# Optimization experiments

Hardware: AMD Instinct MI355X
Metric: run time of the kernel (lower is better)

## Reference

```python
import jax, jax.numpy as jnp
import numpy as np

D_MODEL = 2048
D_STATE = 64
D_HEAD = 64
EXPAND = 2
CHUNK = 256
D_INNER = EXPAND * D_MODEL          # 4096
N_HEADS = D_INNER // D_HEAD          # 64
PARAM_DIM = 1 + 2 * D_STATE          # 129


def setup_inputs() -> dict:
    key = jax.random.key(0)
    k0, k1, k2, k3 = jax.random.split(key, 4)
    x = jax.random.normal(k0, (1, 4096, D_MODEL), jnp.float32)
    w_in = jax.random.normal(k1, (2 * D_INNER, D_MODEL), jnp.float32) * 0.02
    w_param = jax.random.normal(k2, (N_HEADS * PARAM_DIM, D_MODEL), jnp.float32) * 0.02
    w_out = jax.random.normal(k3, (D_MODEL, D_INNER), jnp.float32) * 0.02
    return {"x": x, "w_in": w_in, "w_param": w_param, "w_out": w_out}


def _ssd(a, Bm, Cm, X, Q):
    # a: (nb, l), Bm/Cm: (nb, l, ds), X: (nb, l, dh). Mamba-2 SSD chunked scan.
    nb, l = a.shape
    ds = Bm.shape[-1]
    dh = X.shape[-1]
    nc = l // Q
    la = jnp.log(a).reshape(nb, nc, Q)
    cs = jnp.cumsum(la, axis=-1)                      # cumulative log-decay within chunk
    Bc = Bm.reshape(nb, nc, Q, ds)
    Cc = Cm.reshape(nb, nc, Q, ds)
    Xc = X.reshape(nb, nc, Q, dh)
    # intra-chunk (attention-like dual): L[i,j] = prod_{r=j+1..i} a_r, j<=i
    tri = jnp.tril(jnp.ones((Q, Q), bool))
    L = jnp.where(tri, jnp.exp(cs[..., :, None] - cs[..., None, :]), 0.0)
    scores = jnp.einsum('znid,znjd->znij', Cc, Bc) * L
    y_diag = jnp.einsum('znij,znjh->znih', scores, Xc)
    # per-chunk state contribution: sum_j decay_to_end[j] * B_j^T x_j -> (nb,nc,ds,dh)
    decay_states = jnp.exp(cs[..., -1:] - cs)
    states = jnp.einsum('znj,znjd,znjh->zndh', decay_states, Bc, Xc)
    A_chunk = jnp.exp(cs[..., -1])                    # total decay per chunk (nb, nc)
    def step(S, inp):
        Ac, st = inp
        S_prev = S
        return Ac[:, None, None] * S + st, S_prev
    S0 = jnp.zeros((nb, ds, dh), a.dtype)
    _, S_prev = jax.lax.scan(step, S0, (A_chunk.T, jnp.moveaxis(states, 1, 0)))
    S_prev = jnp.moveaxis(S_prev, 0, 1)               # state entering each chunk (nb,nc,ds,dh)
    y_inter = jnp.einsum('znid,zndh,zni->znih', Cc, S_prev, jnp.exp(cs))
    return (y_diag + y_inter).reshape(nb, l, dh)


def reference(x, w_in, w_param, w_out):
    b, l, _ = x.shape
    xr = x @ w_in.T                                   # (b, l, 2*d_inner)
    inp, res = xr[..., :D_INNER], xr[..., D_INNER:]
    params = (x @ w_param.T).reshape(b, l, N_HEADS, PARAM_DIM)
    dt = jax.nn.softplus(params[..., 0])
    a = jnp.exp(-dt)                                  # (b, l, n_heads)
    Bp = params[..., 1:1 + D_STATE]
    Cp = params[..., 1 + D_STATE:]
    nb = b * N_HEADS
    # NOTE: raw row-major reshapes, mirroring the torch source exactly
    y = _ssd(a.reshape(nb, l),
             Bp.reshape(nb, l, D_STATE),
             Cp.reshape(nb, l, D_STATE),
             inp.reshape(nb, l, D_HEAD),
             CHUNK)
    y = y.reshape(b, l, D_INNER)
    out = y * jax.nn.silu(res)
    return out @ w_out.T
```

## Files before the change

### kernel.cpp

```cpp
#include <hip/hip_runtime.h>
#include <math.h>

#define Q 256

typedef unsigned short u16;
typedef unsigned int u32;
typedef __attribute__((ext_vector_type(8))) short short8;
typedef __attribute__((ext_vector_type(4))) float f32x4;

__device__ __forceinline__ float bf2f(u32 u){
  union { float f; u32 i; } v; v.i = u << 16; return v.f;
}
__device__ __forceinline__ u16 f2bf(float f){
  union { float f; u32 i; } v; v.f = f;
  u32 r = (v.i + 0x7FFFu + ((v.i >> 16) & 1u)) >> 16;
  return (u16)r;
}
__device__ __forceinline__ float softplusf(float x){
  return x > 20.f ? x : log1pf(expf(x));
}
__device__ __forceinline__ float siluf(float x){
  return x / (1.f + expf(-x));
}

__device__ __forceinline__ void gload_lds16(const void* g, const void* l){
  __builtin_amdgcn_global_load_lds(
    (const __attribute__((address_space(1))) void*)(uintptr_t)g,
    (__attribute__((address_space(3))) void*)(u32)(uintptr_t)l,
    16, 0, 0);
}

__device__ __forceinline__ u32 swz_off(int row, int col2){
  return (u32)(row*128 + (col2 ^ ((row & 7) << 4)));
}
__device__ __forceinline__ short8 frag_ld(const u16* buf, int row, int kk, int lk){
  return *(const short8*)((const char*)buf + row*128 + (((kk*4 + lk) ^ (row & 7)) << 4));
}

__global__ __launch_bounds__(256) void cast_bf16(const float* __restrict__ in,
    u16* __restrict__ out)
{
  const size_t i = ((size_t)blockIdx.x * 256 + threadIdx.x) * 4;
  const float4 v = *(const float4*)(in + i);
  ushort4 o;
  o.x = f2bf(v.x); o.y = f2bf(v.y); o.z = f2bf(v.z); o.w = f2bf(v.w);
  *(ushort4*)(out + i) = o;
}

#define MFMA_GEMM_CORE(Abf_, Bbf_, K_) \
  __shared__ short As[128*64]; \
  __shared__ short Bs[128*64]; \
  const int tid = threadIdx.x; \
  const int w = tid >> 6, l = tid & 63; \
  const int m0 = blockIdx.y * 128, n0 = blockIdx.x * 128; \
  const int wr = (w >> 1) * 64, wc = (w & 1) * 64; \
  const int sub = l >> 3; \
  const int scol = ((l & 7) ^ sub) * 8; \
  const int lr16 = l & 15; \
  const int koff = (l >> 4) << 4; \
  const int swz = (l & 7) << 4; \
  f32x4 acc[4][4]; \
  { f32x4 z = {0.f, 0.f, 0.f, 0.f}; \
    _Pragma("unroll") for (int m_ = 0; m_ < 4; m_++) \
    _Pragma("unroll") for (int n_ = 0; n_ < 4; n_++) acc[m_][n_] = z; } \
  const u16* Agp = (Abf_) + (size_t)m0 * (K_); \
  const u16* Bgp = (Bbf_) + (size_t)n0 * (K_); \
  for (int kt = 0; kt < (K_); kt += 64) { \
    __syncthreads(); \
    _Pragma("unroll") for (int i_ = 0; i_ < 4; i_++) { \
      const int rbase = i_*32 + w*8; \
      gload_lds16(Agp + (size_t)(rbase + sub)*(K_) + kt + scol, As + rbase*64); \
      gload_lds16(Bgp + (size_t)(rbase + sub)*(K_) + kt + scol, Bs + rbase*64); \
    } \
    __syncthreads(); \
    short8 af[2][4], bf[2][4]; \
    _Pragma("unroll") for (int kk = 0; kk < 2; kk++) { \
      _Pragma("unroll") for (int m_ = 0; m_ < 4; m_++) \
        af[kk][m_] = *(const short8*)((const char*)As + (wr + m_*16 + lr16)*128 + ((kk*64 + koff) ^ swz)); \
      _Pragma("unroll") for (int n_ = 0; n_ < 4; n_++) \
        bf[kk][n_] = *(const short8*)((const char*)Bs + (wc + n_*16 + lr16)*128 + ((kk*64 + koff) ^ swz)); \
    } \
    _Pragma("unroll") for (int m_ = 0; m_ < 4; m_++) \
    _Pragma("unroll") for (int n_ = 0; n_ < 4; n_++) \
    _Pragma("unroll") for (int kk = 0; kk < 2; kk++) \
      acc[m_][n_] = __builtin_amdgcn_mfma_f32_16x16x32_bf16(af[kk][m_], bf[kk][n_], acc[m_][n_], 0, 0, 0); \
  } \
  const int orow0 = m0 + wr + ((l >> 4) << 2); \
  const int ocol0 = n0 + wc + (l & 15);

__global__ __launch_bounds__(256) void gemm_in(const u16* __restrict__ A,
    const u16* __restrict__ B, u16* __restrict__ inp, u16* __restrict__ resb)
{
  MFMA_GEMM_CORE(A, B, 2048)
  #pragma unroll
  for (int m_ = 0; m_ < 4; m_++)
    #pragma unroll
    for (int n_ = 0; n_ < 4; n_++) {
      const int col = ocol0 + n_*16;
      #pragma unroll
      for (int j = 0; j < 4; j++) {
        const int row = orow0 + m_*16 + j;
        const u16 v = f2bf(acc[m_][n_][j]);
        if (col < 4096) inp[(size_t)row*4096 + col] = v;
        else            resb[(size_t)row*4096 + (col - 4096)] = v;
      }
    }
}

__global__ __launch_bounds__(256) void gemm_par(const u16* __restrict__ A,
    const u16* __restrict__ B, float* __restrict__ dtb,
    u16* __restrict__ Bb, u16* __restrict__ Cb)
{
  MFMA_GEMM_CORE(A, B, 2048)
  #pragma unroll
  for (int m_ = 0; m_ < 4; m_++)
    #pragma unroll
    for (int n_ = 0; n_ < 4; n_++) {
      const int col = ocol0 + n_*16;
      if (col < 8256) {
        const int h = col / 129, rr = col - h*129;
        #pragma unroll
        for (int j = 0; j < 4; j++) {
          const int row = orow0 + m_*16 + j;
          const float v = acc[m_][n_][j];
          if (rr == 0)      dtb[(size_t)row*64 + h] = v;
          else if (rr < 65) Bb[((size_t)row*64 + h)*64 + (rr-1)]  = f2bf(v);
          else              Cb[((size_t)row*64 + h)*64 + (rr-65)] = f2bf(v);
        }
      }
    }
}

__global__ __launch_bounds__(256) void gemm_out(const u16* __restrict__ A,
    const u16* __restrict__ B, float* __restrict__ C)
{
  MFMA_GEMM_CORE(A, B, 4096)
  #pragma unroll
  for (int m_ = 0; m_ < 4; m_++)
    #pragma unroll
    for (int n_ = 0; n_ < 4; n_++) {
      const int col = ocol0 + n_*16;
      #pragma unroll
      for (int j = 0; j < 4; j++)
        C[(size_t)(orow0 + m_*16 + j)*2048 + col] = acc[m_][n_][j];
    }
}

__global__ __launch_bounds__(256) void ssd_phaseA(const float* __restrict__ dtb,
    const u16* __restrict__ Bb, const u16* __restrict__ inp,
    float* __restrict__ cs_g, float* __restrict__ achunk, float* __restrict__ states_t)
{
  const int g = blockIdx.x, tid = threadIdx.x;
  const int p = g * Q + tid;
  __shared__ float sc[Q];
  __shared__ u16 sBt[64*64];
  __shared__ u16 sXt[64*64];
  sc[tid] = -softplusf(dtb[p]);
  __syncthreads();
  for (int off = 1; off < Q; off <<= 1) {
    float v = (tid >= off) ? sc[tid - off] : 0.f;
    __syncthreads();
    if (tid >= off) sc[tid] += v;
    __syncthreads();
  }
  cs_g[p] = sc[tid];
  const float cl = sc[Q-1];
  if (tid == 0) achunk[g] = expf(cl);

  const int w = tid >> 6, l = tid & 63;
  const int lrow = l & 15, lk = l >> 4;
  const int tj = tid & 63, tcb = (tid >> 6) * 16;
  f32x4 acc[4];
  { f32x4 z = {0,0,0,0}; acc[0]=z; acc[1]=z; acc[2]=z; acc[3]=z; }

  for (int js = 0; js < 4; js++) {
    __syncthreads();
    {
      const int jc = js*64 + tj;
      const float wj = expf(cl - sc[jc]);
      const size_t prow = ((size_t)g*Q + jc) * 64;
      union { uint4 v; u16 s[8]; } b0, b1, x0, x1;
      b0.v = *(const uint4*)&Bb[prow + tcb];
      b1.v = *(const uint4*)&Bb[prow + tcb + 8];
      x0.v = *(const uint4*)&inp[prow + tcb];
      x1.v = *(const uint4*)&inp[prow + tcb + 8];
      #pragma unroll
      for (int q = 0; q < 8; q++) {
        const int r0 = tcb + q, r1 = tcb + 8 + q;
        *(u16*)((char*)sBt + swz_off(r0, 2*tj)) = f2bf(wj * bf2f((u32)b0.s[q]));
        *(u16*)((char*)sBt + swz_off(r1, 2*tj)) = f2bf(wj * bf2f((u32)b1.s[q]));
        *(u16*)((char*)sXt + swz_off(r0, 2*tj)) = x0.s[q];
        *(u16*)((char*)sXt + swz_off(r1, 2*tj)) = x1.s[q];
      }
    }
    __syncthreads();
    short8 aX0 = frag_ld(sXt, w*16 + lrow, 0, lk);
    short8 aX1 = frag_ld(sXt, w*16 + lrow, 1, lk);
    #pragma unroll
    for (int n = 0; n < 4; n++) {
      short8 b0 = frag_ld(sBt, n*16 + lrow, 0, lk);
      short8 b1 = frag_ld(sBt, n*16 + lrow, 1, lk);
      acc[n] = __builtin_amdgcn_mfma_f32_16x16x32_bf16(aX0, b0, acc[n], 0, 0, 0);
      acc[n] = __builtin_amdgcn_mfma_f32_16x16x32_bf16(aX1, b1, acc[n], 0, 0, 0);
    }
  }
  #pragma unroll
  for (int reg = 0; reg < 4; reg++) {
    const int d = w*16 + lk*4 + reg;
    #pragma unroll
    for (int n = 0; n < 4; n++)
      states_t[(size_t)g*4096 + d*64 + n*16 + lrow] = acc[n][reg];
  }
}

__global__ __launch_bounds__(256) void ssd_scan(float* __restrict__ states,
    const float* __restrict__ achunk)
{
  const int n = blockIdx.x, tid = threadIdx.x;
  float S[16];
  #pragma unroll
  for (int k = 0; k < 16; k++) S[k] = 0.f;
  for (int c = 0; c < 16; c++) {
    const int g = n*16 + c;
    const float A = achunk[g];
    #pragma unroll
    for (int k = 0; k < 16; k++) {
      const size_t e = (size_t)g * 4096 + tid + k*256;
      const float st = states[e];
      states[e] = S[k];
      S[k] = fmaf(A, S[k], st);
    }
  }
}

__global__ __launch_bounds__(256) void ssd_diag(const u16* __restrict__ Bb,
    const u16* __restrict__ Cb, const u16* __restrict__ inp,
    const float* __restrict__ cs_g, const float* __restrict__ states_t,
    const u16* __restrict__ resb, u16* __restrict__ yb)
{
  const int g = blockIdx.y, it = blockIdx.x, tid = threadIdx.x;
  const int w = tid >> 6, l = tid & 63;
  const int lrow = l & 15, lk = l >> 4;
  const int p_base = g * Q;
  __shared__ u16 sC[64*64];
  __shared__ u16 sB[64*64];
  __shared__ u16 sX[64*64];
  __shared__ u16 sP[64*64];
  __shared__ float csi[64], csj[64];

  const int r = tid >> 2, c0 = (tid & 3) << 4;
  {
    const size_t prow = (size_t)(p_base + it*64 + r) * 64;
    uint4 v0 = *(const uint4*)&Cb[prow + c0];
    uint4 v1 = *(const uint4*)&Cb[prow + c0 + 8];
    *(uint4*)((char*)sC + swz_off(r, c0*2))      = v0;
    *(uint4*)((char*)sC + swz_off(r, c0*2 + 16)) = v1;
    if (tid < 64) csi[tid] = cs_g[p_base + it*64 + tid];
  }
  const int i0 = w * 16;
  const int xj = tid & 63, xdb = (tid >> 6) * 16;
  f32x4 accY[4];
  { f32x4 z = {0,0,0,0}; accY[0]=z; accY[1]=z; accY[2]=z; accY[3]=z; }

  for (int jt = 0; jt <= it; jt++) {
    __syncthreads();
    {
      const size_t prow = (size_t)(p_base + jt*64 + r) * 64;
      uint4 v0 = *(const uint4*)&Bb[prow + c0];
      uint4 v1 = *(const uint4*)&Bb[prow + c0 + 8];
      *(uint4*)((char*)sB + swz_off(r, c0*2))      = v0;
      *(uint4*)((char*)sB + swz_off(r, c0*2 + 16)) = v1;
      if (tid < 64) csj[tid] = cs_g[p_base + jt*64 + tid];
    }
    {
      const size_t prow = (size_t)(p_base + jt*64 + xj) * 64;
      union { uint4 v; u16 s[8]; } x0, x1;
      x0.v = *(const uint4*)&inp[prow + xdb];
      x1.v = *(const uint4*)&inp[prow + xdb + 8];
      #pragma unroll
      for (int q = 0; q < 8; q++) {
        *(u16*)((char*)sX + swz_off(xdb + q,     2*xj)) = x0.s[q];
        *(u16*)((char*)sX + swz_off(xdb + 8 + q, 2*xj)) = x1.s[q];
      }
    }
    __syncthreads();
    f32x4 sAcc[4];
    { f32x4 z = {0,0,0,0}; sAcc[0]=z; sAcc[1]=z; sAcc[2]=z; sAcc[3]=z; }
    {
      short8 aC0 = frag_ld(sC, i0 + lrow, 0, lk);
      short8 aC1 = frag_ld(sC, i0 + lrow, 1, lk);
      #pragma unroll
      for (int n = 0; n < 4; n++) {
        short8 b0 = frag_ld(sB, n*16 + lrow, 0, lk);
        short8 b1 = frag_ld(sB, n*16 + lrow, 1, lk);
        sAcc[n] = __builtin_amdgcn_mfma_f32_16x16x32_bf16(aC0, b0, sAcc[n], 0, 0, 0);
        sAcc[n] = __builtin_amdgcn_mfma_f32_16x16x32_bf16(aC1, b1, sAcc[n], 0, 0, 0);
      }
    }
    const bool full = (jt < it);
    #pragma unroll
    for (int n = 0; n < 4; n++) {
      const int j_l = n*16 + lrow;
      const float cj = csj[j_l];
      #pragma unroll
      for (int reg = 0; reg < 4; reg++) {
        const int i_l = i0 + lk*4 + reg;
        float s = 0.f;
        if (full || j_l <= i_l) s = sAcc[n][reg] * expf(csi[i_l] - cj);
        *(u16*)((char*)sP + swz_off(i_l, n*32 + 2*lrow)) = f2bf(s);
      }
    }
    {
      short8 aP0 = frag_ld(sP, i0 + lrow, 0, lk);
      short8 aP1 = frag_ld(sP, i0 + lrow, 1, lk);
      #pragma unroll
      for (int n = 0; n < 4; n++) {
        short8 x0f = frag_ld(sX, n*16 + lrow, 0, lk);
        short8 x1f = frag_ld(sX, n*16 + lrow, 1, lk);
        accY[n] = __builtin_amdgcn_mfma_f32_16x16x32_bf16(aP0, x0f, accY[n], 0, 0, 0);
        accY[n] = __builtin_amdgcn_mfma_f32_16x16x32_bf16(aP1, x1f, accY[n], 0, 0, 0);
      }
    }
  }
  __syncthreads();
  {
    const int d = tid & 63, sb = (tid >> 6) * 16;
    const float* srow = &states_t[(size_t)g*4096 + d*64 + sb];
    float4 f0 = *(const float4*)(srow);
    float4 f1 = *(const float4*)(srow + 4);
    float4 f2 = *(const float4*)(srow + 8);
    float4 f3 = *(const float4*)(srow + 12);
    union { uint4 v; u16 s[8]; } o0, o1;
    o0.s[0]=f2bf(f0.x); o0.s[1]=f2bf(f0.y); o0.s[2]=f2bf(f0.z); o0.s[3]=f2bf(f0.w);
    o0.s[4]=f2bf(f1.x); o0.s[5]=f2bf(f1.y); o0.s[6]=f2bf(f1.z); o0.s[7]=f2bf(f1.w);
    o1.s[0]=f2bf(f2.x); o1.s[1]=f2bf(f2.y); o1.s[2]=f2bf(f2.z); o1.s[3]=f2bf(f2.w);
    o1.s[4]=f2bf(f3.x); o1.s[5]=f2bf(f3.y); o1.s[6]=f2bf(f3.z); o1.s[7]=f2bf(f3.w);
    *(uint4*)((char*)sB + swz_off(d, sb*2))      = o0.v;
    *(uint4*)((char*)sB + swz_off(d, sb*2 + 16)) = o1.v;
  }
  __syncthreads();
  f32x4 accI[4];
  { f32x4 z = {0,0,0,0}; accI[0]=z; accI[1]=z; accI[2]=z; accI[3]=z; }
  {
    short8 aC0 = frag_ld(sC, i0 + lrow, 0, lk);
    short8 aC1 = frag_ld(sC, i0 + lrow, 1, lk);
    #pragma unroll
    for (int n = 0; n < 4; n++) {
      short8 s0 = frag_ld(sB, n*16 + lrow, 0, lk);
      short8 s1 = frag_ld(sB, n*16 + lrow, 1, lk);
      accI[n] = __builtin_amdgcn_mfma_f32_16x16x32_bf16(aC0, s0, accI[n], 0, 0, 0);
      accI[n] = __builtin_amdgcn_mfma_f32_16x16x32_bf16(aC1, s1, accI[n], 0, 0, 0);
    }
  }
  #pragma unroll
  for (int reg = 0; reg < 4; reg++) {
    const int i_l = i0 + lk*4 + reg;
    const float ei = expf(csi[i_l]);
    const size_t prow = (size_t)(p_base + it*64 + i_l) * 64;
    #pragma unroll
    for (int n = 0; n < 4; n++) {
      const int d = n*16 + lrow;
      const float yv = accY[n][reg] + ei * accI[n][reg];
      const float rv = bf2f((u32)resb[prow + d]);
      yb[prow + d] = f2bf(yv * siluf(rv));
    }
  }
}

extern "C" void kernel_launch(void* const* d_in, const int* in_sizes, int n_in,
                              void* d_out, int out_size, void* d_ws, size_t ws_size,
                              hipStream_t stream)
{
  const float* x       = (const float*)d_in[0];
  const float* w_in    = (const float*)d_in[1];
  const float* w_param = (const float*)d_in[2];
  const float* w_out   = (const float*)d_in[3];
  float* out = (float*)d_out;
  char* ws = (char*)d_ws;

  float* states    = (float*)(ws);
  u16*   xb        = (u16*)  (ws);
  u16*   yb        = (u16*)  (ws + 0x1000000ull);
  u16*   w_in_b    = (u16*)  (ws + 0x1000000ull);
  u16*   w_param_b = (u16*)  (ws + 0x3000000ull);
  u16*   w_out_b   = (u16*)  (ws + 0x5100000ull);
  u16*   inp       = (u16*)  (ws + 0x6100000ull);
  u16*   resb      = (u16*)  (ws + 0x8100000ull);
  u16*   Bb        = (u16*)  (ws + 0xA100000ull);
  u16*   Cb        = (u16*)  (ws + 0xC100000ull);
  float* dtb       = (float*)(ws + 0xE100000ull);
  float* cs        = (float*)(ws + 0xE200000ull);
  float* achunk    = (float*)(ws + 0xE300000ull);

  cast_bf16<<<8192,  256, 0, stream>>>(x, xb);
  cast_bf16<<<16384, 256, 0, stream>>>(w_in, w_in_b);
  cast_bf16<<<16512, 256, 0, stream>>>(w_param, w_param_b);
  cast_bf16<<<8192,  256, 0, stream>>>(w_out, w_out_b);

  gemm_in <<<dim3(64, 32), 256, 0, stream>>>(xb, w_in_b, inp, resb);
  gemm_par<<<dim3(65, 32), 256, 0, stream>>>(xb, w_param_b, dtb, Bb, Cb);
  ssd_phaseA<<<1024, 256, 0, stream>>>(dtb, Bb, inp, cs, achunk, states);
  ssd_scan<<<64, 256, 0, stream>>>(states, achunk);
  ssd_diag<<<dim3(4, 1024), 256, 0, stream>>>(Bb, Cb, inp, cs, states, resb, yb);
  gemm_out<<<dim3(16, 32), 256, 0, stream>>>(yb, w_out_b, out);
}
```

Measured before the change: 652.7 us.

## Replace input and param GEMMs with 256x256-tile multi-stage pipelined MFMA kernel

Replaces the 128x128-tile gemm_in and gemm_par kernels with a new 512-thread GEMM core that uses 256x256 output tiles, a 4-buffer LDS ring (128 KB dynamic shared memory) filled by async global-to-LDS loads issued three stages ahead, and explicit vmcnt waits. It also remaps block IDs across groups of 8 for L2 locality and raises MFMA issue priority. The intent is more operand reuse per tile and overlap of global loads with MFMA work. The cost is heavy register and LDS use, which limits occupancy to about one block per CU, and more padded work on the 8256-wide param GEMM's last tile.

```diff
diff --git a/kernel.cpp b/kernel.cpp
--- a/kernel.cpp
+++ b/kernel.cpp
@@ -45,6 +45,117 @@
   ushort4 o;
   o.x = f2bf(v.x); o.y = f2bf(v.y); o.z = f2bf(v.z); o.w = f2bf(v.w);
   *(ushort4*)(out + i) = o;
+}
+
+#define G256_VM8 asm volatile("s_waitcnt vmcnt(8)" ::: "memory")
+#define G256_VM4 asm volatile("s_waitcnt vmcnt(4)" ::: "memory")
+#define G256_VM0 asm volatile("s_waitcnt vmcnt(0)" ::: "memory")
+
+#define G256_STAGE(s_) \
+  _Pragma("unroll") for (int q = 0; q < 4; q++) \
+    gload_lds16(sptr[q] + (s_)*32, lds + (((s_)&3)*32768) + (q*512 + tid)*16);
+
+#define G256_PHASE(p_, dostage_, VMSTMT) { \
+  const char* sb_ = lds + (((p_)&3)*32768); \
+  short8 af_[8], bf_[4]; \
+  _Pragma("unroll") for (int m = 0; m < 8; m++) af_[m] = *(const short8*)(sb_ + aoff[m]); \
+  _Pragma("unroll") for (int n = 0; n < 4; n++) bf_[n] = *(const short8*)(sb_ + boff[n]); \
+  if (dostage_) { G256_STAGE((p_)+3) } \
+  __builtin_amdgcn_sched_barrier(0); \
+  __builtin_amdgcn_s_setprio(1); \
+  _Pragma("unroll") for (int m = 0; m < 8; m++) \
+  _Pragma("unroll") for (int n = 0; n < 4; n++) \
+    acc[m][n] = __builtin_amdgcn_mfma_f32_16x16x32_bf16(af_[m], bf_[n], acc[m][n], 0, 0, 0); \
+  __builtin_amdgcn_s_setprio(0); \
+  VMSTMT; \
+  __builtin_amdgcn_s_barrier(); \
+  __builtin_amdgcn_sched_barrier(0); \
+}
+
+#define G256_CORE(A_, B_, K_, NTN_) \
+  extern __shared__ char lds[]; \
+  const int tid = threadIdx.x; \
+  const int nwg = gridDim.x, bid = blockIdx.x; \
+  const int wg = (bid & 7) * (nwg >> 3) + (bid >> 3); \
+  const int m0 = (wg / (NTN_)) * 256, n0 = (wg % (NTN_)) * 256; \
+  const int w = tid >> 6, l = tid & 63; \
+  const int wr = w >> 2, wc = w & 3; \
+  const int lr = l & 15, lk = l >> 4; \
+  const u16* sptr[4]; \
+  _Pragma("unroll") for (int q = 0; q < 4; q++) { \
+    const int c = q*512 + tid; \
+    const int r = c >> 3; \
+    const int jl = (c & 7) ^ (r & 7); \
+    sptr[q] = (jl < 4) ? ((A_) + (size_t)(m0 + r)*(K_) + jl*8) \
+                       : ((B_) + (size_t)(n0 + r)*(K_) + (jl-4)*8); \
+  } \
+  int aoff[8], boff[4]; \
+  _Pragma("unroll") for (int m = 0; m < 8; m++) { \
+    const int r = wr*128 + m*16 + lr; \
+    aoff[m] = r*128 + ((lk ^ (r & 7)) << 4); } \
+  _Pragma("unroll") for (int n = 0; n < 4; n++) { \
+    const int r = wc*64 + n*16 + lr; \
+    boff[n] = r*128 + (((4 + lk) ^ (r & 7)) << 4); } \
+  f32x4 acc[8][4]; \
+  { f32x4 z = {0.f,0.f,0.f,0.f}; \
+    _Pragma("unroll") for (int m = 0; m < 8; m++) \
+    _Pragma("unroll") for (int n = 0; n < 4; n++) acc[m][n] = z; } \
+  G256_STAGE(0) G256_STAGE(1) G256_STAGE(2) \
+  G256_VM8; \
+  __builtin_amdgcn_s_barrier(); \
+  __builtin_amdgcn_sched_barrier(0); \
+  { const int NPH = (K_)/32; \
+    for (int p = 0; p < NPH-4; p += 2) { \
+      G256_PHASE(p,   1, G256_VM8) \
+      G256_PHASE(p+1, 1, G256_VM8) \
+    } \
+    G256_PHASE(NPH-4, 1, G256_VM8) \
+    G256_PHASE(NPH-3, 0, G256_VM4) \
+    G256_PHASE(NPH-2, 0, G256_VM0) \
+    G256_PHASE(NPH-1, 0, (void)0) \
+  }
+
+__global__ void __launch_bounds__(512, 2) gemm_in256(const u16* __restrict__ A,
+    const u16* __restrict__ B, u16* __restrict__ inp, u16* __restrict__ resb)
+{
+  G256_CORE(A, B, 2048, 32)
+  #pragma unroll
+  for (int m = 0; m < 8; m++)
+    #pragma unroll
+    for (int n = 0; n < 4; n++) {
+      const int col = n0 + wc*64 + n*16 + lr;
+      #pragma unroll
+      for (int j = 0; j < 4; j++) {
+        const int row = m0 + wr*128 + m*16 + lk*4 + j;
+        const u16 v = f2bf(acc[m][n][j]);
+        if (col < 4096) inp[(size_t)row*4096 + col] = v;
+        else            resb[(size_t)row*4096 + (col - 4096)] = v;
+      }
+    }
+}
+
+__global__ void __launch_bounds__(512, 2) gemm_par256(const u16* __restrict__ A,
+    const u16* __restrict__ B, float* __restrict__ dtb,
+    u16* __restrict__ Bb, u16* __restrict__ Cb)
+{
+  G256_CORE(A, B, 2048, 33)
+  #pragma unroll
+  for (int m = 0; m < 8; m++)
+    #pragma unroll
+    for (int n = 0; n < 4; n++) {
+      const int col = n0 + wc*64 + n*16 + lr;
+      if (col < 8256) {
+        const int h = col / 129, rr = col - h*129;
+        #pragma unroll
+        for (int j = 0; j < 4; j++) {
+          const int row = m0 + wr*128 + m*16 + lk*4 + j;
+          const float v = acc[m][n][j];
+          if (rr == 0)      dtb[(size_t)row*64 + h] = v;
+          else if (rr < 65) Bb[((size_t)row*64 + h)*64 + (rr-1)]  = f2bf(v);
+          else              Cb[((size_t)row*64 + h)*64 + (rr-65)] = f2bf(v);
+        }
+      }
+    }
 }
 
 #define MFMA_GEMM_CORE(Abf_, Bbf_, K_) \
@@ -88,49 +199,6 @@
   const int orow0 = m0 + wr + ((l >> 4) << 2); \
   const int ocol0 = n0 + wc + (l & 15);
 
-__global__ __launch_bounds__(256) void gemm_in(const u16* __restrict__ A,
-    const u16* __restrict__ B, u16* __restrict__ inp, u16* __restrict__ resb)
-{
-  MFMA_GEMM_CORE(A, B, 2048)
-  #pragma unroll
-  for (int m_ = 0; m_ < 4; m_++)
-    #pragma unroll
-    for (int n_ = 0; n_ < 4; n_++) {
-      const int col = ocol0 + n_*16;
-      #pragma unroll
-      for (int j = 0; j < 4; j++) {
-        const int row = orow0 + m_*16 + j;
-        const u16 v = f2bf(acc[m_][n_][j]);
-        if (col < 4096) inp[(size_t)row*4096 + col] = v;
-        else            resb[(size_t)row*4096 + (col - 4096)] = v;
-      }
-    }
-}
-
-__global__ __launch_bounds__(256) void gemm_par(const u16* __restrict__ A,
-    const u16* __restrict__ B, float* __restrict__ dtb,
-    u16* __restrict__ Bb, u16* __restrict__ Cb)
-{
-  MFMA_GEMM_CORE(A, B, 2048)
-  #pragma unroll
-  for (int m_ = 0; m_ < 4; m_++)
-    #pragma unroll
-    for (int n_ = 0; n_ < 4; n_++) {
-      const int col = ocol0 + n_*16;
-      if (col < 8256) {
-        const int h = col / 129, rr = col - h*129;
-        #pragma unroll
-        for (int j = 0; j < 4; j++) {
-          const int row = orow0 + m_*16 + j;
-          const float v = acc[m_][n_][j];
-          if (rr == 0)      dtb[(size_t)row*64 + h] = v;
-          else if (rr < 65) Bb[((size_t)row*64 + h)*64 + (rr-1)]  = f2bf(v);
-          else              Cb[((size_t)row*64 + h)*64 + (rr-65)] = f2bf(v);
-        }
-      }
-    }
-}
-
 __global__ __launch_bounds__(256) void gemm_out(const u16* __restrict__ A,
     const u16* __restrict__ B, float* __restrict__ C)
 {
@@ -392,13 +460,18 @@
   float* cs        = (float*)(ws + 0xE200000ull);
   float* achunk    = (float*)(ws + 0xE300000ull);
 
+  hipFuncSetAttribute((const void*)gemm_in256,
+      hipFuncAttributeMaxDynamicSharedMemorySize, 131072);
+  hipFuncSetAttribute((const void*)gemm_par256,
+      hipFuncAttributeMaxDynamicSharedMemorySize, 131072);
+
   cast_bf16<<<8192,  256, 0, stream>>>(x, xb);
   cast_bf16<<<16384, 256, 0, stream>>>(w_in, w_in_b);
   cast_bf16<<<16512, 256, 0, stream>>>(w_param, w_param_b);
   cast_bf16<<<8192,  256, 0, stream>>>(w_out, w_out_b);
 
-  gemm_in <<<dim3(64, 32), 256, 0, stream>>>(xb, w_in_b, inp, resb);
-  gemm_par<<<dim3(65, 32), 256, 0, stream>>>(xb, w_param_b, dtb, Bb, Cb);
+  gemm_in256 <<<512, 512, 131072, stream>>>(xb, w_in_b, inp, resb);
+  gemm_par256<<<528, 512, 131072, stream>>>(xb, w_param_b, dtb, Bb, Cb);
   ssd_phaseA<<<1024, 256, 0, stream>>>(dtb, Bb, inp, cs, achunk, states);
   ssd_scan<<<64, 256, 0, stream>>>(states, achunk);
   ssd_diag<<<dim3(4, 1024), 256, 0, stream>>>(Bb, Cb, inp, cs, states, resb, yb);
```

Result: faster. 566.2 us (-13.2%).

## Rewrite GEMMs as double-buffered 128x256 tiles and merge cast kernels

Applied to the files above, without the earlier changes.

Replaces the 128x128 single-buffered MFMA GEMM core with a 512-thread 128x256 tile core. It uses K-steps of 32, double-buffered LDS loads that overlap the next stage's global-to-LDS copy with the current MFMAs, XCD-aware block remapping, and s_setprio around the MFMA section. The four fp32-to-bf16 cast launches are merged into one kernel that dispatches by index range. This aims to cut LDS sync stalls and launch overhead and to improve operand reuse, at the cost of more LDS per block and a grid of 1056 for gemm_par, where padded tiles do wasted work.

```diff
diff --git a/kernel.cpp b/kernel.cpp
--- a/kernel.cpp
+++ b/kernel.cpp
@@ -37,92 +37,122 @@
   return *(const short8*)((const char*)buf + row*128 + (((kk*4 + lk) ^ (row & 7)) << 4));
 }
 
-__global__ __launch_bounds__(256) void cast_bf16(const float* __restrict__ in,
-    u16* __restrict__ out)
-{
-  const size_t i = ((size_t)blockIdx.x * 256 + threadIdx.x) * 4;
-  const float4 v = *(const float4*)(in + i);
+__global__ __launch_bounds__(256) void cast_all(const float* __restrict__ x,
+    const float* __restrict__ w_in, const float* __restrict__ w_param,
+    const float* __restrict__ w_out, u16* __restrict__ xb,
+    u16* __restrict__ w_in_b, u16* __restrict__ w_param_b, u16* __restrict__ w_out_b)
+{
+  const size_t g = (size_t)blockIdx.x * 256 + threadIdx.x;
+  const float* src; u16* dst; size_t off;
+  if (g < 2097152)        { src = x;       dst = xb;        off = g; }
+  else if (g < 6291456)   { src = w_in;    dst = w_in_b;    off = g - 2097152; }
+  else if (g < 10518528)  { src = w_param; dst = w_param_b; off = g - 6291456; }
+  else                    { src = w_out;   dst = w_out_b;   off = g - 10518528; }
+  const float4 v = *(const float4*)(src + off*4);
   ushort4 o;
   o.x = f2bf(v.x); o.y = f2bf(v.y); o.z = f2bf(v.z); o.w = f2bf(v.w);
-  *(ushort4*)(out + i) = o;
-}
-
-#define MFMA_GEMM_CORE(Abf_, Bbf_, K_) \
-  __shared__ short As[128*64]; \
-  __shared__ short Bs[128*64]; \
+  *(ushort4*)(dst + off*4) = o;
+}
+
+#define T256_STAGE(s_) \
+  _Pragma("unroll") for (int q = 0; q < 3; q++) \
+    gload_lds16(sptr[q] + (s_)*32, lds + (((s_)&1)*24576) + (q*512 + tid)*16);
+
+#define T256_CORE(A_, B_, K_, NTN_) \
+  __shared__ char lds[49152]; \
   const int tid = threadIdx.x; \
+  const int nwg = gridDim.x, bid = blockIdx.x; \
+  const int wg = (bid & 7) * (nwg >> 3) + (bid >> 3); \
+  const int m0 = (wg / (NTN_)) * 128, n0 = (wg % (NTN_)) * 256; \
   const int w = tid >> 6, l = tid & 63; \
-  const int m0 = blockIdx.y * 128, n0 = blockIdx.x * 128; \
-  const int wr = (w >> 1) * 64, wc = (w & 1) * 64; \
-  const int sub = l >> 3; \
-  const int scol = ((l & 7) ^ sub) * 8; \
-  const int lr16 = l & 15; \
-  const int koff = (l >> 4) << 4; \
-  const int swz = (l & 7) << 4; \
+  const int wr = w >> 2, wc = w & 3; \
+  const int lr = l & 15, lk = l >> 4; \
+  const u16* sptr[3]; \
+  _Pragma("unroll") for (int q = 0; q < 3; q++) { \
+    const int c = q*512 + tid; \
+    const int r = c >> 3; \
+    const int lg = (c & 7) ^ (r & 7); \
+    const int lrow2 = 2*r + (lg >> 2); \
+    const int kc = lg & 3; \
+    sptr[q] = (lrow2 < 128) ? ((A_) + (size_t)(m0 + lrow2)*(K_) + kc*8) \
+                            : ((B_) + (size_t)(n0 + (lrow2 - 128))*(K_) + kc*8); \
+  } \
+  const int arow0 = wr*64 + lr; \
+  const int abrow = arow0 >> 1; \
+  const int abase = abrow*128 + ((((arow0 & 1)*4 + lk) ^ (abrow & 7)) << 4); \
+  const int brow0 = 64 + ((wc*64 + lr) >> 1); \
+  const int bbase = brow0*128 + ((((lr & 1)*4 + lk) ^ (brow0 & 7)) << 4); \
   f32x4 acc[4][4]; \
-  { f32x4 z = {0.f, 0.f, 0.f, 0.f}; \
-    _Pragma("unroll") for (int m_ = 0; m_ < 4; m_++) \
-    _Pragma("unroll") for (int n_ = 0; n_ < 4; n_++) acc[m_][n_] = z; } \
-  const u16* Agp = (Abf_) + (size_t)m0 * (K_); \
-  const u16* Bgp = (Bbf_) + (size_t)n0 * (K_); \
-  for (int kt = 0; kt < (K_); kt += 64) { \
-    __syncthreads(); \
-    _Pragma("unroll") for (int i_ = 0; i_ < 4; i_++) { \
-      const int rbase = i_*32 + w*8; \
-      gload_lds16(Agp + (size_t)(rbase + sub)*(K_) + kt + scol, As + rbase*64); \
-      gload_lds16(Bgp + (size_t)(rbase + sub)*(K_) + kt + scol, Bs + rbase*64); \
+  { f32x4 z = {0.f,0.f,0.f,0.f}; \
+    _Pragma("unroll") for (int m = 0; m < 4; m++) \
+    _Pragma("unroll") for (int n = 0; n < 4; n++) acc[m][n] = z; } \
+  T256_STAGE(0) \
+  asm volatile("s_waitcnt vmcnt(0)" ::: "memory"); \
+  __builtin_amdgcn_s_barrier(); \
+  { const int NS = (K_)/32; \
+    for (int s = 0; s < NS-1; ++s) { \
+      const char* sb_ = lds + ((s & 1)*24576); \
+      short8 aF[4], bF[4]; \
+      T256_STAGE(s+1) \
+      _Pragma("unroll") for (int m = 0; m < 4; m++) \
+        aF[m] = *(const short8*)(sb_ + abase + m*1024); \
+      _Pragma("unroll") for (int n = 0; n < 4; n++) \
+        bF[n] = *(const short8*)(sb_ + bbase + n*1024); \
+      __builtin_amdgcn_s_setprio(1); \
+      _Pragma("unroll") for (int m = 0; m < 4; m++) \
+      _Pragma("unroll") for (int n = 0; n < 4; n++) \
+        acc[m][n] = __builtin_amdgcn_mfma_f32_16x16x32_bf16(aF[m], bF[n], acc[m][n], 0, 0, 0); \
+      __builtin_amdgcn_s_setprio(0); \
+      asm volatile("s_waitcnt vmcnt(0)" ::: "memory"); \
+      __builtin_amdgcn_s_barrier(); \
     } \
-    __syncthreads(); \
-    short8 af[2][4], bf[2][4]; \
-    _Pragma("unroll") for (int kk = 0; kk < 2; kk++) { \
-      _Pragma("unroll") for (int m_ = 0; m_ < 4; m_++) \
-        af[kk][m_] = *(const short8*)((const char*)As + (wr + m_*16 + lr16)*128 + ((kk*64 + koff) ^ swz)); \
-      _Pragma("unroll") for (int n_ = 0; n_ < 4; n_++) \
-        bf[kk][n_] = *(const short8*)((const char*)Bs + (wc + n_*16 + lr16)*128 + ((kk*64 + koff) ^ swz)); \
+    { const char* sb_ = lds + (((K_)/32 - 1) & 1)*24576; \
+      short8 aF[4], bF[4]; \
+      _Pragma("unroll") for (int m = 0; m < 4; m++) \
+        aF[m] = *(const short8*)(sb_ + abase + m*1024); \
+      _Pragma("unroll") for (int n = 0; n < 4; n++) \
+        bF[n] = *(const short8*)(sb_ + bbase + n*1024); \
+      _Pragma("unroll") for (int m = 0; m < 4; m++) \
+      _Pragma("unroll") for (int n = 0; n < 4; n++) \
+        acc[m][n] = __builtin_amdgcn_mfma_f32_16x16x32_bf16(aF[m], bF[n], acc[m][n], 0, 0, 0); \
     } \
-    _Pragma("unroll") for (int m_ = 0; m_ < 4; m_++) \
-    _Pragma("unroll") for (int n_ = 0; n_ < 4; n_++) \
-    _Pragma("unroll") for (int kk = 0; kk < 2; kk++) \
-      acc[m_][n_] = __builtin_amdgcn_mfma_f32_16x16x32_bf16(af[kk][m_], bf[kk][n_], acc[m_][n_], 0, 0, 0); \
-  } \
-  const int orow0 = m0 + wr + ((l >> 4) << 2); \
-  const int ocol0 = n0 + wc + (l & 15);
-
-__global__ __launch_bounds__(256) void gemm_in(const u16* __restrict__ A,
+  }
+
+__global__ void __launch_bounds__(512, 4) gemm_in256(const u16* __restrict__ A,
     const u16* __restrict__ B, u16* __restrict__ inp, u16* __restrict__ resb)
 {
-  MFMA_GEMM_CORE(A, B, 2048)
-  #pragma unroll
-  for (int m_ = 0; m_ < 4; m_++)
-    #pragma unroll
-    for (int n_ = 0; n_ < 4; n_++) {
-      const int col = ocol0 + n_*16;
+  T256_CORE(A, B, 2048, 32)
+  #pragma unroll
+  for (int m = 0; m < 4; m++)
+    #pragma unroll
+    for (int n = 0; n < 4; n++) {
+      const int col = n0 + wc*64 + n*16 + lr;
       #pragma unroll
       for (int j = 0; j < 4; j++) {
-        const int row = orow0 + m_*16 + j;
-        const u16 v = f2bf(acc[m_][n_][j]);
+        const int row = m0 + wr*64 + m*16 + lk*4 + j;
+        const u16 v = f2bf(acc[m][n][j]);
         if (col < 4096) inp[(size_t)row*4096 + col] = v;
         else            resb[(size_t)row*4096 + (col - 4096)] = v;
       }
     }
 }
 
-__global__ __launch_bounds__(256) void gemm_par(const u16* __restrict__ A,
+__global__ void __launch_bounds__(512, 4) gemm_par256(const u16* __restrict__ A,
     const u16* __restrict__ B, float* __restrict__ dtb,
     u16* __restrict__ Bb, u16* __restrict__ Cb)
 {
-  MFMA_GEMM_CORE(A, B, 2048)
-  #pragma unroll
-  for (int m_ = 0; m_ < 4; m_++)
-    #pragma unroll
-    for (int n_ = 0; n_ < 4; n_++) {
-      const int col = ocol0 + n_*16;
+  T256_CORE(A, B, 2048, 33)
+  #pragma unroll
+  for (int m = 0; m < 4; m++)
+    #pragma unroll
+    for (int n = 0; n < 4; n++) {
+      const int col = n0 + wc*64 + n*16 + lr;
       if (col < 8256) {
         const int h = col / 129, rr = col - h*129;
         #pragma unroll
         for (int j = 0; j < 4; j++) {
-          const int row = orow0 + m_*16 + j;
-          const float v = acc[m_][n_][j];
+          const int row = m0 + wr*64 + m*16 + lk*4 + j;
+          const float v = acc[m][n][j];
           if (rr == 0)      dtb[(size_t)row*64 + h] = v;
           else if (rr < 65) Bb[((size_t)row*64 + h)*64 + (rr-1)]  = f2bf(v);
           else              Cb[((size_t)row*64 + h)*64 + (rr-65)] = f2bf(v);
@@ -131,18 +161,18 @@
     }
 }
 
-__global__ __launch_bounds__(256) void gemm_out(const u16* __restrict__ A,
+__global__ void __launch_bounds__(512, 4) gemm_out256(const u16* __restrict__ A,
     const u16* __restrict__ B, float* __restrict__ C)
 {
-  MFMA_GEMM_CORE(A, B, 4096)
-  #pragma unroll
-  for (int m_ = 0; m_ < 4; m_++)
-    #pragma unroll
-    for (int n_ = 0; n_ < 4; n_++) {
-      const int col = ocol0 + n_*16;
+  T256_CORE(A, B, 4096, 8)
+  #pragma unroll
+  for (int m = 0; m < 4; m++)
+    #pragma unroll
+    for (int n = 0; n < 4; n++) {
+      const int col = n0 + wc*64 + n*16 + lr;
       #pragma unroll
       for (int j = 0; j < 4; j++)
-        C[(size_t)(orow0 + m_*16 + j)*2048 + col] = acc[m_][n_][j];
+        C[(size_t)(m0 + wr*64 + m*16 + lk*4 + j)*2048 + col] = acc[m][n][j];
     }
 }
 
@@ -392,15 +422,13 @@
   float* cs        = (float*)(ws + 0xE200000ull);
   float* achunk    = (float*)(ws + 0xE300000ull);
 
-  cast_bf16<<<8192,  256, 0, stream>>>(x, xb);
-  cast_bf16<<<16384, 256, 0, stream>>>(w_in, w_in_b);
-  cast_bf16<<<16512, 256, 0, stream>>>(w_param, w_param_b);
-  cast_bf16<<<8192,  256, 0, stream>>>(w_out, w_out_b);
-
-  gemm_in <<<dim3(64, 32), 256, 0, stream>>>(xb, w_in_b, inp, resb);
-  gemm_par<<<dim3(65, 32), 256, 0, stream>>>(xb, w_param_b, dtb, Bb, Cb);
+  cast_all<<<49280, 256, 0, stream>>>(x, w_in, w_param, w_out,
+                                      xb, w_in_b, w_param_b, w_out_b);
+
+  gemm_in256 <<<1024, 512, 0, stream>>>(xb, w_in_b, inp, resb);
+  gemm_par256<<<1056, 512, 0, stream>>>(xb, w_param_b, dtb, Bb, Cb);
   ssd_phaseA<<<1024, 256, 0, stream>>>(dtb, Bb, inp, cs, achunk, states);
   ssd_scan<<<64, 256, 0, stream>>>(states, achunk);
   ssd_diag<<<dim3(4, 1024), 256, 0, stream>>>(Bb, Cb, inp, cs, states, resb, yb);
-  gemm_out<<<dim3(16, 32), 256, 0, stream>>>(yb, w_out_b, out);
-}
+  gemm_out256<<<256, 512, 0, stream>>>(yb, w_out_b, out);
+}
```

Result: faster. 561.9 us (-13.9%).
